# Performance work log

Hardware: AMD Instinct MI355X
Metric: run time of the kernel (lower is better)

The kernel has to match this reference:

```python
import jax, jax.numpy as jnp
import numpy as np

D_MODEL = 1024
NHEAD = 16
DFF = 4096
B, S = 4, 1024
EPS = 1e-5  # torch LayerNorm default


def _layernorm(x, g, b):
    mu = jnp.mean(x, axis=-1, keepdims=True)
    var = jnp.mean((x - mu) ** 2, axis=-1, keepdims=True)
    return (x - mu) * jax.lax.rsqrt(var + EPS) * g + b


def setup_inputs() -> dict:
    key = jax.random.key(0)
    ks = jax.random.split(key, 12)
    sc = 0.02
    d, h, f = D_MODEL, NHEAD, DFF
    return {
        "src": jax.random.normal(ks[0], (B, S, d), dtype=jnp.float32),
        "w_in": jax.random.normal(ks[1], (3 * d, d), dtype=jnp.float32) * sc,  # packed q,k,v proj (torch in_proj_weight)
        "b_in": jnp.zeros((3 * d,), jnp.float32),
        "w_out": jax.random.normal(ks[2], (d, d), dtype=jnp.float32) * sc,
        "b_out": jnp.zeros((d,), jnp.float32),
        "w1": jax.random.normal(ks[3], (f, d), dtype=jnp.float32) * sc,
        "b1": jnp.zeros((f,), jnp.float32),
        "w2": jax.random.normal(ks[4], (d, f), dtype=jnp.float32) * sc,
        "b2": jnp.zeros((d,), jnp.float32),
        "g1": jnp.ones((d,), jnp.float32),
        "be1": jnp.zeros((d,), jnp.float32),
        "g2": jnp.ones((d,), jnp.float32),
        "be2": jnp.zeros((d,), jnp.float32),
    }


def reference(src, w_in, b_in, w_out, b_out, w1, b1, w2, b2, g1, be1, g2, be2):
    # dropout layers are identity in eval mode
    b, s, d = src.shape
    h = NHEAD
    dh = d // h
    # --- MHA, need_weights=True, average_attn_weights=False ---
    qkv = src @ w_in.T + b_in                      # [B,S,3D]
    q, k, v = jnp.split(qkv, 3, axis=-1)
    q = q.reshape(b, s, h, dh).transpose(0, 2, 1, 3) * (1.0 / np.sqrt(dh))
    k = k.reshape(b, s, h, dh).transpose(0, 2, 1, 3)
    v = v.reshape(b, s, h, dh).transpose(0, 2, 1, 3)
    scores = jnp.einsum("bhqd,bhkd->bhqk", q, k)   # [B,H,S,S]
    attn_weights = jax.nn.softmax(scores, axis=-1)  # per-head weights, materialized
    ctx = jnp.einsum("bhqk,bhkd->bhqd", attn_weights, v)
    ctx = ctx.transpose(0, 2, 1, 3).reshape(b, s, d)
    attn_out = ctx @ w_out.T + b_out
    # --- residual + LN1 ---
    x = _layernorm(src + attn_out, g1, be1)
    # --- FFN ---
    ff = jax.nn.relu(x @ w1.T + b1) @ w2.T + b2
    # --- residual + LN2 ---
    out = _layernorm(x + ff, g2, be2)
    return out, attn_weights
```

## Files before the change

kernel.cpp:

```cpp
#include <hip/hip_runtime.h>


#define DEVI __device__ __forceinline__

typedef __attribute__((ext_vector_type(4))) float f4;
typedef __attribute__((ext_vector_type(4))) float f32x4;
typedef __attribute__((ext_vector_type(8))) short s8;
typedef __attribute__((ext_vector_type(4))) unsigned short us4;
typedef unsigned short u16;

DEVI short bf16r(float f) {
  unsigned u = __builtin_bit_cast(unsigned, f);
  unsigned r = (u + 0x7fffu + ((u >> 16) & 1u)) >> 16;
  return (short)(unsigned short)r;
}
DEVI float bf2f(u16 h) {
  unsigned u = ((unsigned)h) << 16;
  return __builtin_bit_cast(float, u);
}
DEVI s8 cvt8(f4 a, f4 b) {
  s8 r;
  r[0] = bf16r(a.x); r[1] = bf16r(a.y); r[2] = bf16r(a.z); r[3] = bf16r(a.w);
  r[4] = bf16r(b.x); r[5] = bf16r(b.y); r[6] = bf16r(b.z); r[7] = bf16r(b.w);
  return r;
}

DEVI void gload16(const void* g, void* l) {
  __builtin_amdgcn_global_load_lds(
      (const __attribute__((address_space(1))) unsigned int*)g,
      (__attribute__((address_space(3))) unsigned int*)l, 16, 0, 0);
}

template<int BM, int BN, bool A32, bool OUTBF16>
__global__ __launch_bounds__(256)
void gemm(const void* __restrict__ Ap_, long lda, long sAh, long sAl,
          const u16* __restrict__ Bp_, long ldb, long sBh, long sBl,
          void* __restrict__ Cp_, long ldc, long sCh, long sCl, int inner,
          const float* __restrict__ bias, int K,
          int qcols, float qscale, int do_relu)
{
  constexpr int WM = BM / 2, WN = BN / 2, FM = WM / 16, FN = WN / 16;
  constexpr int CA = BM / 32, CB = BN / 32;
  __shared__ __align__(128) short As[BM * 64];
  __shared__ __align__(128) short Bs[BN * 64];

  int z = blockIdx.z, zh = z / inner, zl = z - zh * inner;
  long aoff = (long)zh * sAh + (long)zl * sAl;
  long coff = (long)zh * sCh + (long)zl * sCl;

  int row0 = blockIdx.y * BM, col0 = blockIdx.x * BN;
  int tid = threadIdx.x, lane = tid & 63, w = tid >> 6;
  int wr = w >> 1, wc = w & 1;

  const u16* Bb = Bp_ + (long)zh * sBh + (long)zl * sBl + (long)col0 * ldb;
  const u16* Ab16 = nullptr;
  const float* Ab32 = nullptr;
  if constexpr (A32) Ab32 = (const float*)Ap_ + aoff + (long)row0 * lda;
  else               Ab16 = (const u16*)Ap_ + aoff + (long)row0 * lda;

  f32x4 acc[FM][FN] = {};

  for (int k0 = 0; k0 < K; k0 += 64) {
    if (k0) __syncthreads();
    if constexpr (A32) {
      int r = tid >> 1, half = tid & 1;
      const float* gp = Ab32 + (long)r * lda + k0 + half * 32;
      char* lb = (char*)As + r * 128;
#pragma unroll
      for (int gi = 0; gi < 4; ++gi) {
        f4 v0 = *(const f4*)(gp + gi * 8);
        f4 v1 = *(const f4*)(gp + gi * 8 + 4);
        int g = half * 4 + gi;
        *(s8*)(lb + ((g ^ (r & 7)) * 16)) = cvt8(v0, v1);
      }
    } else {
#pragma unroll
      for (int c = 0; c < CA; ++c) {
        int seg = w * CA + c;
        int r = seg * 8 + (lane >> 3);
        int g = (lane & 7) ^ (r & 7);
        gload16(Ab16 + (long)r * lda + k0 + g * 8, (char*)As + seg * 1024);
      }
    }
#pragma unroll
    for (int c = 0; c < CB; ++c) {
      int seg = w * CB + c;
      int r = seg * 8 + (lane >> 3);
      int g = (lane & 7) ^ (r & 7);
      gload16(Bb + (long)r * ldb + k0 + g * 8, (char*)Bs + seg * 1024);
    }
    __syncthreads();

#pragma unroll
    for (int kk = 0; kk < 2; ++kk) {
      s8 af[FM], bf[FN];
      int lr = lane & 15, kg = kk * 4 + (lane >> 4);
#pragma unroll
      for (int i = 0; i < FM; ++i) {
        int R = wr * WM + i * 16 + lr;
        af[i] = *(const s8*)((char*)As + R * 128 + ((kg ^ (R & 7)) * 16));
      }
#pragma unroll
      for (int j = 0; j < FN; ++j) {
        int R = wc * WN + j * 16 + lr;
        bf[j] = *(const s8*)((char*)Bs + R * 128 + ((kg ^ (R & 7)) * 16));
      }
#pragma unroll
      for (int i = 0; i < FM; ++i)
#pragma unroll
        for (int j = 0; j < FN; ++j)
          acc[i][j] = __builtin_amdgcn_mfma_f32_16x16x32_bf16(af[i], bf[j], acc[i][j], 0, 0, 0);
    }
  }

  float* Cf = (float*)Cp_ + coff;
  u16*   Cb = (u16*)Cp_ + coff;
#pragma unroll
  for (int i = 0; i < FM; ++i) {
#pragma unroll
    for (int j = 0; j < FN; ++j) {
      int rb = row0 + wr * WM + i * 16 + (lane >> 4) * 4;
      int c  = col0 + wc * WN + j * 16 + (lane & 15);
      float bv = bias ? bias[c] : 0.0f;
      float sc = (c < qcols) ? qscale : 1.0f;
#pragma unroll
      for (int q = 0; q < 4; ++q) {
        float v = (acc[i][j][q] + bv) * sc;
        if (do_relu) v = fmaxf(v, 0.0f);
        long idx = (long)(rb + q) * ldc + c;
        if constexpr (OUTBF16) Cb[idx] = (u16)bf16r(v);
        else                   Cf[idx] = v;
      }
    }
  }
}

__global__ __launch_bounds__(256)
void attn_fused(const u16* __restrict__ qkvb, const u16* __restrict__ vtb,
                float* __restrict__ attnW, u16* __restrict__ ctxb)
{
  __shared__ __align__(128) u16 Kt[128 * 64];
  __shared__ __align__(128) u16 Vt[64 * 128];
  __shared__ __align__(128) u16 Pt[4 * 32 * 128];

  int blk = blockIdx.x;
  int bh = blk >> 3, qt = blk & 7;
  int b = bh >> 4, h = bh & 15;
  int tid = threadIdx.x, lane = tid & 63, w = tid >> 6;

  const u16* Qg = qkvb + (long)b * 3145728 + (long)(qt * 128) * 3072 + h * 64;
#pragma unroll
  for (int c = 0; c < 4; ++c) {
    int seg = w * 4 + c;
    int r = seg * 8 + (lane >> 3);
    int g = (lane & 7) ^ (r & 7);
    gload16(Qg + (long)r * 3072 + g * 8, (char*)Kt + seg * 1024);
  }
  __syncthreads();
  s8 aq[2][2];
#pragma unroll
  for (int i = 0; i < 2; ++i)
#pragma unroll
    for (int kk = 0; kk < 2; ++kk) {
      int R = w * 32 + i * 16 + (lane & 15);
      int kg = kk * 4 + (lane >> 4);
      aq[i][kk] = *(const s8*)((char*)Kt + R * 128 + ((kg ^ (R & 7)) * 16));
    }

  const u16* Kbase = qkvb + (long)b * 3145728 + 1024 + h * 64;
  const u16* Vbase = vtb + (long)bh * 65536;

  float m[2][4], l[2][4];
#pragma unroll
  for (int i = 0; i < 2; ++i)
#pragma unroll
    for (int q = 0; q < 4; ++q) { m[i][q] = -1e30f; l[i][q] = 0.0f; }

  for (int kc = 0; kc < 8; ++kc) {
    __syncthreads();
#pragma unroll
    for (int c = 0; c < 4; ++c) {
      int seg = w * 4 + c;
      int r = seg * 8 + (lane >> 3);
      int g = (lane & 7) ^ (r & 7);
      gload16(Kbase + (long)(kc * 128 + r) * 3072 + g * 8, (char*)Kt + seg * 1024);
    }
    __syncthreads();

    f32x4 s[2][8] = {};
#pragma unroll
    for (int kk = 0; kk < 2; ++kk) {
      s8 bk[8];
      int kg = kk * 4 + (lane >> 4);
#pragma unroll
      for (int j = 0; j < 8; ++j) {
        int R = j * 16 + (lane & 15);
        bk[j] = *(const s8*)((char*)Kt + R * 128 + ((kg ^ (R & 7)) * 16));
      }
#pragma unroll
      for (int i = 0; i < 2; ++i)
#pragma unroll
        for (int j = 0; j < 8; ++j)
          s[i][j] = __builtin_amdgcn_mfma_f32_16x16x32_bf16(aq[i][kk], bk[j], s[i][j], 0, 0, 0);
    }

#pragma unroll
    for (int i = 0; i < 2; ++i)
#pragma unroll
      for (int q = 0; q < 4; ++q) {
        float mx = s[i][0][q];
#pragma unroll
        for (int j = 1; j < 8; ++j) mx = fmaxf(mx, s[i][j][q]);
        mx = fmaxf(mx, __shfl_xor(mx, 1));
        mx = fmaxf(mx, __shfl_xor(mx, 2));
        mx = fmaxf(mx, __shfl_xor(mx, 4));
        mx = fmaxf(mx, __shfl_xor(mx, 8));
        float mn = fmaxf(m[i][q], mx);
        float sum = 0.0f;
#pragma unroll
        for (int j = 0; j < 8; ++j) sum += __expf(s[i][j][q] - mn);
        sum += __shfl_xor(sum, 1);
        sum += __shfl_xor(sum, 2);
        sum += __shfl_xor(sum, 4);
        sum += __shfl_xor(sum, 8);
        l[i][q] = l[i][q] * __expf(m[i][q] - mn) + sum;
        m[i][q] = mn;
      }
  }

  float inv[2][4];
#pragma unroll
  for (int i = 0; i < 2; ++i)
#pragma unroll
    for (int q = 0; q < 4; ++q) inv[i][q] = 1.0f / l[i][q];

  f32x4 o_[2][4] = {};
  float* aw = attnW + (long)bh * 1048576 + (long)(qt * 128) * 1024;
  u16* Pw = Pt + w * 4096;

  for (int kc = 0; kc < 8; ++kc) {
    __syncthreads();
#pragma unroll
    for (int c = 0; c < 4; ++c) {
      int seg = w * 4 + c;
      int r = seg * 8 + (lane >> 3);
      int g = (lane & 7) ^ (r & 7);
      gload16(Kbase + (long)(kc * 128 + r) * 3072 + g * 8, (char*)Kt + seg * 1024);
    }
#pragma unroll
    for (int c = 0; c < 4; ++c) {
      int seg = w * 4 + c;
      int r = seg * 4 + (lane >> 4);
      int g = (lane & 15) ^ (r & 7);
      gload16(Vbase + (long)r * 1024 + kc * 128 + g * 8, (char*)Vt + seg * 1024);
    }
    __syncthreads();

    f32x4 s[2][8] = {};
#pragma unroll
    for (int kk = 0; kk < 2; ++kk) {
      s8 bk[8];
      int kg = kk * 4 + (lane >> 4);
#pragma unroll
      for (int j = 0; j < 8; ++j) {
        int R = j * 16 + (lane & 15);
        bk[j] = *(const s8*)((char*)Kt + R * 128 + ((kg ^ (R & 7)) * 16));
      }
#pragma unroll
      for (int i = 0; i < 2; ++i)
#pragma unroll
        for (int j = 0; j < 8; ++j)
          s[i][j] = __builtin_amdgcn_mfma_f32_16x16x32_bf16(aq[i][kk], bk[j], s[i][j], 0, 0, 0);
    }

#pragma unroll
    for (int i = 0; i < 2; ++i)
#pragma unroll
      for (int j = 0; j < 8; ++j)
#pragma unroll
        for (int q = 0; q < 4; ++q) {
          float p = __expf(s[i][j][q] - m[i][q]) * inv[i][q];
          int R = i * 16 + (lane >> 4) * 4 + q;
          int C = j * 16 + (lane & 15);
          aw[(long)(w * 32 + R) * 1024 + kc * 128 + C] = p;
          *(u16*)((char*)Pw + R * 256 + (((C >> 3) ^ (R & 7)) * 16) + (C & 7) * 2)
              = (u16)bf16r(p);
        }

#pragma unroll
    for (int kks = 0; kks < 4; ++kks) {
      int kg = kks * 4 + (lane >> 4);
      s8 pa[2], bv[4];
#pragma unroll
      for (int i = 0; i < 2; ++i) {
        int R = i * 16 + (lane & 15);
        pa[i] = *(const s8*)((char*)Pw + R * 256 + ((kg ^ (R & 7)) * 16));
      }
#pragma unroll
      for (int j = 0; j < 4; ++j) {
        int R = j * 16 + (lane & 15);
        bv[j] = *(const s8*)((char*)Vt + R * 256 + ((kg ^ (R & 7)) * 16));
      }
#pragma unroll
      for (int i = 0; i < 2; ++i)
#pragma unroll
        for (int j = 0; j < 4; ++j)
          o_[i][j] = __builtin_amdgcn_mfma_f32_16x16x32_bf16(pa[i], bv[j], o_[i][j], 0, 0, 0);
    }
  }

#pragma unroll
  for (int i = 0; i < 2; ++i)
#pragma unroll
    for (int j = 0; j < 4; ++j)
#pragma unroll
      for (int q = 0; q < 4; ++q) {
        int R = w * 32 + i * 16 + (lane >> 4) * 4 + q;
        int col = h * 64 + j * 16 + (lane & 15);
        ctxb[(long)(b * 1024 + qt * 128 + R) * 1024 + col] = (u16)bf16r(o_[i][j][q]);
      }
}

DEVI float blockSum(float v, float* sh) {
#pragma unroll
  for (int o = 32; o > 0; o >>= 1) v += __shfl_xor(v, o);
  int w = threadIdx.x >> 6;
  __syncthreads();
  if ((threadIdx.x & 63) == 0) sh[w] = v;
  __syncthreads();
  return (sh[0] + sh[1]) + (sh[2] + sh[3]);
}

template<bool RBF16>
__global__ __launch_bounds__(256)
void ln_combine(const float* __restrict__ P0, const float* __restrict__ P1,
                const void* __restrict__ resid, const float* __restrict__ bias,
                const float* __restrict__ g, const float* __restrict__ be,
                float* __restrict__ outf, u16* __restrict__ outb)
{
  __shared__ float sh[4];
  long row = blockIdx.x;
  int t = threadIdx.x;
  long off = row * 1024 + t * 4;
  f4 v = *(const f4*)(P0 + off);
  v += *(const f4*)(P1 + off);
  if constexpr (RBF16) {
    us4 rp = *(const us4*)((const u16*)resid + off);
    v.x += bf2f(rp.x); v.y += bf2f(rp.y); v.z += bf2f(rp.z); v.w += bf2f(rp.w);
  } else {
    v += *(const f4*)((const float*)resid + off);
  }
  v += *(const f4*)(bias + t * 4);
  float s = (v.x + v.y) + (v.z + v.w);
  s = blockSum(s, sh);
  float mu = s * (1.0f / 1024.0f);
  f4 d = v - mu;
  float s2 = (d.x * d.x + d.y * d.y) + (d.z * d.z + d.w * d.w);
  s2 = blockSum(s2, sh);
  float rs = rsqrtf(s2 * (1.0f / 1024.0f) + 1e-5f);
  f4 gg = *(const f4*)(g + t * 4);
  f4 bb = *(const f4*)(be + t * 4);
  f4 o = d * rs * gg + bb;
  if (outf) *(f4*)(outf + off) = o;
  if (outb) {
    us4 ob;
    ob.x = (u16)bf16r(o.x); ob.y = (u16)bf16r(o.y);
    ob.z = (u16)bf16r(o.z); ob.w = (u16)bf16r(o.w);
    *(us4*)(outb + off) = ob;
  }
}

__global__ __launch_bounds__(256)
void cvt_all(const float* __restrict__ s0, const float* __restrict__ s1,
             const float* __restrict__ s2, const float* __restrict__ s3,
             const float* __restrict__ s4,
             u16* __restrict__ d0, u16* __restrict__ d1, u16* __restrict__ d2,
             u16* __restrict__ d3, u16* __restrict__ d4)
{
  int bi = blockIdx.x;
  const float* s; u16* d; int base;
  if      (bi < 2048) { s = s0; d = d0; base = bi; }
  else if (bi < 3584) { s = s1; d = d1; base = bi - 2048; }
  else if (bi < 4096) { s = s2; d = d2; base = bi - 3584; }
  else if (bi < 6144) { s = s3; d = d3; base = bi - 4096; }
  else                { s = s4; d = d4; base = bi - 6144; }
  long i = ((long)base * 256 + threadIdx.x) * 8;
  f4 a = *(const f4*)(s + i);
  f4 b = *(const f4*)(s + i + 4);
  *(s8*)(d + i) = cvt8(a, b);
}

__global__ __launch_bounds__(256)
void transpose_v(const u16* __restrict__ qkv, u16* __restrict__ vt) {
  __shared__ u16 tile[64][72];
  int blk = blockIdx.x, bh = blk >> 4, st = blk & 15;
  int b = bh >> 4, h = bh & 15, s0 = st * 64;
  const u16* gq = qkv + (long)b * 1024 * 3072 + 2048 + (long)h * 64;
  int t = threadIdx.x;
  int sl = t >> 4, dq = (t & 15) * 4;
#pragma unroll
  for (int it = 0; it < 4; ++it) {
    int s = it * 16 + sl;
    us4 v = *(const us4*)(gq + (long)(s0 + s) * 3072 + dq);
    tile[dq + 0][s] = v.x; tile[dq + 1][s] = v.y;
    tile[dq + 2][s] = v.z; tile[dq + 3][s] = v.w;
  }
  __syncthreads();
  u16* o = vt + (long)bh * 65536 + s0;
  int dl = t >> 4, sq = (t & 15) * 4;
#pragma unroll
  for (int it = 0; it < 4; ++it) {
    int d = it * 16 + dl;
    us4 v;
    v.x = tile[d][sq + 0]; v.y = tile[d][sq + 1];
    v.z = tile[d][sq + 2]; v.w = tile[d][sq + 3];
    *(us4*)(o + (long)d * 1024 + sq) = v;
  }
}

extern "C" void kernel_launch(void* const* d_in, const int* in_sizes, int n_in,
                              void* d_out, int out_size, void* d_ws, size_t ws_size,
                              hipStream_t stream)
{
  (void)in_sizes; (void)n_in; (void)out_size; (void)ws_size;
  const float* src   = (const float*)d_in[0];
  const float* w_in  = (const float*)d_in[1];
  const float* b_in  = (const float*)d_in[2];
  const float* w_out = (const float*)d_in[3];
  const float* b_out = (const float*)d_in[4];
  const float* w1    = (const float*)d_in[5];
  const float* b1    = (const float*)d_in[6];
  const float* w2    = (const float*)d_in[7];
  const float* b2    = (const float*)d_in[8];
  const float* g1    = (const float*)d_in[9];
  const float* be1   = (const float*)d_in[10];
  const float* g2    = (const float*)d_in[11];
  const float* be2   = (const float*)d_in[12];

  float* out   = (float*)d_out;
  float* attnW = out + (long)4 * 1024 * 1024;

  char* ws = (char*)d_ws;
  u16*   qkvb   = (u16*)(ws);
  u16*   vtb    = (u16*)(ws + 25165824);
  u16*   h1b    = (u16*)(ws);
  u16*   srcb   = (u16*)(ws + 33554432);
  u16*   w_in_b = (u16*)(ws + 41943040);
  u16*   w_outb = (u16*)(ws + 48234496);
  u16*   w1b    = (u16*)(ws + 50331648);
  u16*   w2b    = (u16*)(ws + 58720256);
  float* P0     = (float*)(ws + 67108864);
  float* P1     = (float*)(ws + 83886080);
  u16*   ctxb   = (u16*)(ws + 100663296);
  u16*   xb     = (u16*)(ws + 109051904);

  cvt_all<<<dim3(8192), 256, 0, stream>>>(src, w_in, w_out, w1, w2,
                                          srcb, w_in_b, w_outb, w1b, w2b);

  gemm<128, 128, false, true><<<dim3(24, 32, 1), 256, 0, stream>>>(
      srcb, 1024, 0, 0, w_in_b, 1024, 0, 0, qkvb, 3072, 0, 0, 1,
      b_in, 1024, 1024, 0.125f, 0);

  transpose_v<<<dim3(1024), 256, 0, stream>>>(qkvb, vtb);

  attn_fused<<<dim3(512), 256, 0, stream>>>(qkvb, vtb, attnW, ctxb);

  gemm<128, 128, false, false><<<dim3(8, 32, 2), 256, 0, stream>>>(
      ctxb, 1024, 0, 512, w_outb, 1024, 0, 512,
      P0, 1024, 0, 4194304, 2,
      nullptr, 512, 0, 1.0f, 0);

  ln_combine<false><<<dim3(4096), 256, 0, stream>>>(
      P0, P1, src, b_out, g1, be1, nullptr, xb);

  gemm<128, 128, false, true><<<dim3(32, 32, 1), 256, 0, stream>>>(
      xb, 1024, 0, 0, w1b, 1024, 0, 0, h1b, 4096, 0, 0, 1,
      b1, 1024, 0, 1.0f, 1);

  gemm<128, 128, false, false><<<dim3(8, 32, 2), 256, 0, stream>>>(
      h1b, 4096, 0, 2048, w2b, 4096, 0, 2048,
      P0, 1024, 0, 4194304, 2,
      nullptr, 2048, 0, 1.0f, 0);

  ln_combine<true><<<dim3(4096), 256, 0, stream>>>(
      P0, P1, xb, b2, g2, be2, out, nullptr);
}
```

Baseline: 331.7 us.

## Replace GEMMs with 256x256-tile triple-buffered 512-thread kernel and split-K of 4

Swaps the 128x128 GEMM for a 256x256-tile, 8-wave kernel. It uses a three-slot LDS ring with K-steps of 32, manual waitcnt and barrier scheduling, and raised priority around the MFMA bursts. The goal is more data reuse per tile and overlap of global loads with compute. The out-projection and FFN2 GEMMs now split K four ways instead of two, and the two LayerNorm passes sum four partial buffers. The workspace is rearranged so the partials reuse buffers that are already dead. The trade-offs: fewer blocks for the QKV and FFN1 GEMMs (192 and 256 blocks), which may underfill the CUs, plus extra partial-sum traffic.

Result: no change. 329.9 us (-0.5%).

```diff
diff --git a/kernel.cpp b/kernel.cpp
--- a/kernel.cpp
+++ b/kernel.cpp
@@ -31,101 +31,123 @@
       (__attribute__((address_space(3))) unsigned int*)l, 16, 0, 0);
 }
 
-template<int BM, int BN, bool A32, bool OUTBF16>
-__global__ __launch_bounds__(256)
-void gemm(const void* __restrict__ Ap_, long lda, long sAh, long sAl,
-          const u16* __restrict__ Bp_, long ldb, long sBh, long sBl,
-          void* __restrict__ Cp_, long ldc, long sCh, long sCl, int inner,
-          const float* __restrict__ bias, int K,
-          int qcols, float qscale, int do_relu)
+#define BAR()   __builtin_amdgcn_s_barrier()
+#define LGKM0() do { asm volatile("s_waitcnt lgkmcnt(0)" ::: "memory"); \
+                     __builtin_amdgcn_sched_barrier(0); } while (0)
+#define VM4()   do { asm volatile("s_waitcnt vmcnt(4)" ::: "memory"); \
+                     __builtin_amdgcn_sched_barrier(0); } while (0)
+
+template<bool OUTBF16>
+__global__ __launch_bounds__(512, 2)
+void gemm256(const u16* __restrict__ A, long lda, long sA,
+             const u16* __restrict__ B, long ldb, long sB,
+             void* __restrict__ Cp, long ldc,
+             long c0, long c1, long c2, long c3,
+             const float* __restrict__ bias, int K,
+             int qcols, float qscale, int do_relu)
 {
-  constexpr int WM = BM / 2, WN = BN / 2, FM = WM / 16, FN = WN / 16;
-  constexpr int CA = BM / 32, CB = BN / 32;
-  __shared__ __align__(128) short As[BM * 64];
-  __shared__ __align__(128) short Bs[BN * 64];
-
-  int z = blockIdx.z, zh = z / inner, zl = z - zh * inner;
-  long aoff = (long)zh * sAh + (long)zl * sAl;
-  long coff = (long)zh * sCh + (long)zl * sCl;
-
-  int row0 = blockIdx.y * BM, col0 = blockIdx.x * BN;
-  int tid = threadIdx.x, lane = tid & 63, w = tid >> 6;
-  int wr = w >> 1, wc = w & 1;
-
-  const u16* Bb = Bp_ + (long)zh * sBh + (long)zl * sBl + (long)col0 * ldb;
-  const u16* Ab16 = nullptr;
-  const float* Ab32 = nullptr;
-  if constexpr (A32) Ab32 = (const float*)Ap_ + aoff + (long)row0 * lda;
-  else               Ab16 = (const u16*)Ap_ + aoff + (long)row0 * lda;
-
-  f32x4 acc[FM][FN] = {};
-
-  for (int k0 = 0; k0 < K; k0 += 64) {
-    if (k0) __syncthreads();
-    if constexpr (A32) {
-      int r = tid >> 1, half = tid & 1;
-      const float* gp = Ab32 + (long)r * lda + k0 + half * 32;
-      char* lb = (char*)As + r * 128;
-#pragma unroll
-      for (int gi = 0; gi < 4; ++gi) {
-        f4 v0 = *(const f4*)(gp + gi * 8);
-        f4 v1 = *(const f4*)(gp + gi * 8 + 4);
-        int g = half * 4 + gi;
-        *(s8*)(lb + ((g ^ (r & 7)) * 16)) = cvt8(v0, v1);
-      }
-    } else {
-#pragma unroll
-      for (int c = 0; c < CA; ++c) {
-        int seg = w * CA + c;
-        int r = seg * 8 + (lane >> 3);
-        int g = (lane & 7) ^ (r & 7);
-        gload16(Ab16 + (long)r * lda + k0 + g * 8, (char*)As + seg * 1024);
-      }
-    }
-#pragma unroll
-    for (int c = 0; c < CB; ++c) {
-      int seg = w * CB + c;
-      int r = seg * 8 + (lane >> 3);
-      int g = (lane & 7) ^ (r & 7);
-      gload16(Bb + (long)r * ldb + k0 + g * 8, (char*)Bs + seg * 1024);
-    }
-    __syncthreads();
-
-#pragma unroll
-    for (int kk = 0; kk < 2; ++kk) {
-      s8 af[FM], bf[FN];
-      int lr = lane & 15, kg = kk * 4 + (lane >> 4);
-#pragma unroll
-      for (int i = 0; i < FM; ++i) {
-        int R = wr * WM + i * 16 + lr;
-        af[i] = *(const s8*)((char*)As + R * 128 + ((kg ^ (R & 7)) * 16));
-      }
-#pragma unroll
-      for (int j = 0; j < FN; ++j) {
-        int R = wc * WN + j * 16 + lr;
-        bf[j] = *(const s8*)((char*)Bs + R * 128 + ((kg ^ (R & 7)) * 16));
-      }
-#pragma unroll
-      for (int i = 0; i < FM; ++i)
-#pragma unroll
-        for (int j = 0; j < FN; ++j)
-          acc[i][j] = __builtin_amdgcn_mfma_f32_16x16x32_bf16(af[i], bf[j], acc[i][j], 0, 0, 0);
-    }
-  }
-
-  float* Cf = (float*)Cp_ + coff;
-  u16*   Cb = (u16*)Cp_ + coff;
-#pragma unroll
-  for (int i = 0; i < FM; ++i) {
-#pragma unroll
-    for (int j = 0; j < FN; ++j) {
-      int rb = row0 + wr * WM + i * 16 + (lane >> 4) * 4;
-      int c  = col0 + wc * WN + j * 16 + (lane & 15);
+  __shared__ __align__(128) char LDS[98304];
+
+  const int tid = threadIdx.x, lane = tid & 63, w = tid >> 6;
+  const int wr = w >> 2, wc = w & 3;
+  const int z = blockIdx.z;
+  const int row0 = blockIdx.y * 256, col0 = blockIdx.x * 256;
+
+  const u16* Ag = A + (long)z * sA + (long)row0 * lda;
+  const u16* Bg = B + (long)z * sB + (long)col0 * ldb;
+  long coff = (z == 0) ? c0 : (z == 1) ? c1 : (z == 2) ? c2 : c3;
+
+  const int NT = K >> 5;
+
+  const int sr = (w << 4) + (lane >> 2);
+  const int gsrc = (lane & 3) ^ ((sr >> 1) & 3);
+
+  auto stageA = [&](int kt, int slot) {
+#pragma unroll
+    for (int h = 0; h < 2; ++h)
+      gload16(Ag + (long)(h * 128 + sr) * lda + kt * 32 + gsrc * 8,
+              LDS + slot * 16384 + h * 8192 + (w << 10));
+  };
+  auto stageB = [&](int kt, int slot) {
+#pragma unroll
+    for (int h = 0; h < 2; ++h)
+      gload16(Bg + (long)(h * 128 + sr) * ldb + kt * 32 + gsrc * 8,
+              LDS + 49152 + slot * 16384 + h * 8192 + (w << 10));
+  };
+
+  const int kg = lane >> 4, lr = lane & 15;
+  auto rdA = [&](int buf, int fig, s8* aF) {
+#pragma unroll
+    for (int i = 0; i < 4; ++i) {
+      int R = wr * 128 + (fig * 4 + i) * 16 + lr;
+      aF[i] = *(const s8*)(LDS + buf * 16384 + R * 64 + ((kg ^ ((R >> 1) & 3)) << 4));
+    }
+  };
+  auto rdB = [&](int buf, s8* bF) {
+#pragma unroll
+    for (int j = 0; j < 4; ++j) {
+      int R = wc * 64 + j * 16 + lr;
+      bF[j] = *(const s8*)(LDS + 49152 + buf * 16384 + R * 64 + ((kg ^ ((R >> 1) & 3)) << 4));
+    }
+  };
+
+  f32x4 acc[8][4] = {};
+
+  stageA(0, 0); stageB(0, 0);
+  stageA(1, 1); stageB(1, 1);
+  VM4();
+  BAR();
+
+  int buf = 0;
+  for (int t = 0; t < NT; ++t) {
+    int nbuf = buf + 2; if (nbuf >= 3) nbuf -= 3;
+    int tc = (t + 2 < NT) ? t + 2 : NT - 1;
+    s8 aF[4], bF[4], aG[4];
+
+    rdB(buf, bF);
+    rdA(buf, 0, aF);
+    stageA(tc, nbuf);
+    BAR();
+    LGKM0();
+    __builtin_amdgcn_s_setprio(1);
+#pragma unroll
+    for (int i = 0; i < 4; ++i)
+#pragma unroll
+      for (int j = 0; j < 4; ++j)
+        acc[i][j] = __builtin_amdgcn_mfma_f32_16x16x32_bf16(aF[i], bF[j], acc[i][j], 0, 0, 0);
+    __builtin_amdgcn_s_setprio(0);
+    BAR();
+
+    rdA(buf, 1, aG);
+    stageB(tc, nbuf);
+    BAR();
+    LGKM0();
+    __builtin_amdgcn_s_setprio(1);
+#pragma unroll
+    for (int i = 0; i < 4; ++i)
+#pragma unroll
+      for (int j = 0; j < 4; ++j)
+        acc[4 + i][j] = __builtin_amdgcn_mfma_f32_16x16x32_bf16(aG[i], bF[j], acc[4 + i][j], 0, 0, 0);
+    __builtin_amdgcn_s_setprio(0);
+    VM4();
+    BAR();
+    buf = (buf == 2) ? 0 : buf + 1;
+  }
+  asm volatile("s_waitcnt vmcnt(0)" ::: "memory");
+
+  float* Cf = (float*)Cp + coff;
+  u16*   Cb = (u16*)Cp + coff;
+#pragma unroll
+  for (int fi = 0; fi < 8; ++fi) {
+#pragma unroll
+    for (int fj = 0; fj < 4; ++fj) {
+      int rb = row0 + wr * 128 + fi * 16 + (lane >> 4) * 4;
+      int c  = col0 + wc * 64 + fj * 16 + lr;
       float bv = bias ? bias[c] : 0.0f;
       float sc = (c < qcols) ? qscale : 1.0f;
 #pragma unroll
       for (int q = 0; q < 4; ++q) {
-        float v = (acc[i][j][q] + bv) * sc;
+        float v = (acc[fi][fj][q] + bv) * sc;
         if (do_relu) v = fmaxf(v, 0.0f);
         long idx = (long)(rb + q) * ldc + c;
         if constexpr (OUTBF16) Cb[idx] = (u16)bf16r(v);
@@ -163,8 +185,8 @@
 #pragma unroll
     for (int kk = 0; kk < 2; ++kk) {
       int R = w * 32 + i * 16 + (lane & 15);
-      int kg = kk * 4 + (lane >> 4);
-      aq[i][kk] = *(const s8*)((char*)Kt + R * 128 + ((kg ^ (R & 7)) * 16));
+      int kgq = kk * 4 + (lane >> 4);
+      aq[i][kk] = *(const s8*)((char*)Kt + R * 128 + ((kgq ^ (R & 7)) * 16));
     }
 
   const u16* Kbase = qkvb + (long)b * 3145728 + 1024 + h * 64;
@@ -191,11 +213,11 @@
 #pragma unroll
     for (int kk = 0; kk < 2; ++kk) {
       s8 bk[8];
-      int kg = kk * 4 + (lane >> 4);
+      int kgq = kk * 4 + (lane >> 4);
 #pragma unroll
       for (int j = 0; j < 8; ++j) {
         int R = j * 16 + (lane & 15);
-        bk[j] = *(const s8*)((char*)Kt + R * 128 + ((kg ^ (R & 7)) * 16));
+        bk[j] = *(const s8*)((char*)Kt + R * 128 + ((kgq ^ (R & 7)) * 16));
       }
 #pragma unroll
       for (int i = 0; i < 2; ++i)
@@ -260,11 +282,11 @@
 #pragma unroll
     for (int kk = 0; kk < 2; ++kk) {
       s8 bk[8];
-      int kg = kk * 4 + (lane >> 4);
+      int kgq = kk * 4 + (lane >> 4);
 #pragma unroll
       for (int j = 0; j < 8; ++j) {
         int R = j * 16 + (lane & 15);
-        bk[j] = *(const s8*)((char*)Kt + R * 128 + ((kg ^ (R & 7)) * 16));
+        bk[j] = *(const s8*)((char*)Kt + R * 128 + ((kgq ^ (R & 7)) * 16));
       }
 #pragma unroll
       for (int i = 0; i < 2; ++i)
@@ -289,17 +311,17 @@
 
 #pragma unroll
     for (int kks = 0; kks < 4; ++kks) {
-      int kg = kks * 4 + (lane >> 4);
+      int kgq = kks * 4 + (lane >> 4);
       s8 pa[2], bv[4];
 #pragma unroll
       for (int i = 0; i < 2; ++i) {
         int R = i * 16 + (lane & 15);
-        pa[i] = *(const s8*)((char*)Pw + R * 256 + ((kg ^ (R & 7)) * 16));
+        pa[i] = *(const s8*)((char*)Pw + R * 256 + ((kgq ^ (R & 7)) * 16));
       }
 #pragma unroll
       for (int j = 0; j < 4; ++j) {
         int R = j * 16 + (lane & 15);
-        bv[j] = *(const s8*)((char*)Vt + R * 256 + ((kg ^ (R & 7)) * 16));
+        bv[j] = *(const s8*)((char*)Vt + R * 256 + ((kgq ^ (R & 7)) * 16));
       }
 #pragma unroll
       for (int i = 0; i < 2; ++i)
@@ -333,10 +355,11 @@
 
 template<bool RBF16>
 __global__ __launch_bounds__(256)
-void ln_combine(const float* __restrict__ P0, const float* __restrict__ P1,
-                const void* __restrict__ resid, const float* __restrict__ bias,
-                const float* __restrict__ g, const float* __restrict__ be,
-                float* __restrict__ outf, u16* __restrict__ outb)
+void ln_combine4(const float* __restrict__ P0, const float* __restrict__ P1,
+                 const float* __restrict__ P2, const float* __restrict__ P3,
+                 const void* __restrict__ resid, const float* __restrict__ bias,
+                 const float* __restrict__ g, const float* __restrict__ be,
+                 float* __restrict__ outf, u16* __restrict__ outb)
 {
   __shared__ float sh[4];
   long row = blockIdx.x;
@@ -344,6 +367,8 @@
   long off = row * 1024 + t * 4;
   f4 v = *(const f4*)(P0 + off);
   v += *(const f4*)(P1 + off);
+  v += *(const f4*)(P2 + off);
+  v += *(const f4*)(P3 + off);
   if constexpr (RBF16) {
     us4 rp = *(const us4*)((const u16*)resid + off);
     v.x += bf2f(rp.x); v.y += bf2f(rp.y); v.z += bf2f(rp.z); v.w += bf2f(rp.w);
@@ -443,45 +468,44 @@
   char* ws = (char*)d_ws;
   u16*   qkvb   = (u16*)(ws);
   u16*   vtb    = (u16*)(ws + 25165824);
+  u16*   srcb   = (u16*)(ws + 33554432);
+  u16*   ctxb   = (u16*)(ws + 41943040);
+  u16*   xb     = (u16*)(ws + 50331648);
+  u16*   w_in_b = (u16*)(ws + 58720256);
+  u16*   w_outb = (u16*)(ws + 65011712);
+  u16*   w1b    = (u16*)(ws + 67108864);
+  u16*   w2b    = (u16*)(ws + 75497472);
   u16*   h1b    = (u16*)(ws);
-  u16*   srcb   = (u16*)(ws + 33554432);
-  u16*   w_in_b = (u16*)(ws + 41943040);
-  u16*   w_outb = (u16*)(ws + 48234496);
-  u16*   w1b    = (u16*)(ws + 50331648);
-  u16*   w2b    = (u16*)(ws + 58720256);
-  float* P0     = (float*)(ws + 67108864);
-  float* P1     = (float*)(ws + 83886080);
-  u16*   ctxb   = (u16*)(ws + 100663296);
-  u16*   xb     = (u16*)(ws + 109051904);
+  const long Q0 = 0,        Q1 = 4194304,  Q2 = 20971520, Q3 = 25165824;
+  const long R0 = 8388608,  R1 = 14680064, R2 = 20971520, R3 = 25165824;
+  float* wsf = (float*)ws;
 
   cvt_all<<<dim3(8192), 256, 0, stream>>>(src, w_in, w_out, w1, w2,
                                           srcb, w_in_b, w_outb, w1b, w2b);
 
-  gemm<128, 128, false, true><<<dim3(24, 32, 1), 256, 0, stream>>>(
-      srcb, 1024, 0, 0, w_in_b, 1024, 0, 0, qkvb, 3072, 0, 0, 1,
+  gemm256<true><<<dim3(12, 16, 1), 512, 0, stream>>>(
+      srcb, 1024, 0, w_in_b, 1024, 0, qkvb, 3072, 0, 0, 0, 0,
       b_in, 1024, 1024, 0.125f, 0);
 
   transpose_v<<<dim3(1024), 256, 0, stream>>>(qkvb, vtb);
 
   attn_fused<<<dim3(512), 256, 0, stream>>>(qkvb, vtb, attnW, ctxb);
 
-  gemm<128, 128, false, false><<<dim3(8, 32, 2), 256, 0, stream>>>(
-      ctxb, 1024, 0, 512, w_outb, 1024, 0, 512,
-      P0, 1024, 0, 4194304, 2,
-      nullptr, 512, 0, 1.0f, 0);
-
-  ln_combine<false><<<dim3(4096), 256, 0, stream>>>(
-      P0, P1, src, b_out, g1, be1, nullptr, xb);
-
-  gemm<128, 128, false, true><<<dim3(32, 32, 1), 256, 0, stream>>>(
-      xb, 1024, 0, 0, w1b, 1024, 0, 0, h1b, 4096, 0, 0, 1,
+  gemm256<false><<<dim3(4, 16, 4), 512, 0, stream>>>(
+      ctxb, 1024, 256, w_outb, 1024, 256, wsf, 1024, Q0, Q1, Q2, Q3,
+      nullptr, 256, 0, 1.0f, 0);
+
+  ln_combine4<false><<<dim3(4096), 256, 0, stream>>>(
+      wsf + Q0, wsf + Q1, wsf + Q2, wsf + Q3, src, b_out, g1, be1, nullptr, xb);
+
+  gemm256<true><<<dim3(16, 16, 1), 512, 0, stream>>>(
+      xb, 1024, 0, w1b, 1024, 0, h1b, 4096, 0, 0, 0, 0,
       b1, 1024, 0, 1.0f, 1);
 
-  gemm<128, 128, false, false><<<dim3(8, 32, 2), 256, 0, stream>>>(
-      h1b, 4096, 0, 2048, w2b, 4096, 0, 2048,
-      P0, 1024, 0, 4194304, 2,
-      nullptr, 2048, 0, 1.0f, 0);
-
-  ln_combine<true><<<dim3(4096), 256, 0, stream>>>(
-      P0, P1, xb, b2, g2, be2, out, nullptr);
-}
+  gemm256<false><<<dim3(4, 16, 4), 512, 0, stream>>>(
+      h1b, 4096, 1024, w2b, 4096, 1024, wsf, 1024, R0, R1, R2, R3,
+      nullptr, 1024, 0, 1.0f, 0);
+
+  ln_combine4<true><<<dim3(4096), 256, 0, stream>>>(
+      wsf + R0, wsf + R1, wsf + R2, wsf + R3, xb, b2, g2, be2, out, nullptr);
+}
```
